# Optimization experiments

Hardware: AMD Instinct MI355X
Metric: run time of the kernel (lower is better)

## Reference

```python
import jax, jax.numpy as jnp
import numpy as np

DT = 0.1
DX = 1.0
DY = 1.0
NUM_STEPS = 5
EPS = 1e-06


def _smooth3(c):
    # replicate-pad 3-tap mean filter along last axis (matches F.pad replicate + conv1d)
    cp = jnp.concatenate([c[..., :1], c, c[..., -1:]], axis=-1)
    return (cp[..., :-2] + cp[..., 1:-1] + cp[..., 2:]) / 3.0


def _thomas(a, b, c, d):
    # a, b, c, d: (M, N). Batched Thomas solve, sequential recurrence over N via lax.scan.
    M, N = d.shape
    a0 = a.at[:, 0].set(0.0)  # a[:,0] unused; zero it so the first scan step gives c0/(b0+eps)

    def fwd(carry, inp):
        c_prev, d_prev = carry
        ai, bi, ci, di = inp
        denom = bi - ai * c_prev + EPS
        cs = ci / denom
        ds = (di - ai * d_prev) / denom
        return (cs, ds), (cs, ds)

    init = (jnp.zeros((M,), d.dtype), jnp.zeros((M,), d.dtype))
    _, (c_star, d_star) = jax.lax.scan(fwd, init, (a0.T, b.T, c.T, d.T))  # (N, M)

    def bwd(x_next, inp):
        cs, ds = inp
        x = ds - cs * x_next
        return x, x

    x_last = d_star[-1]
    _, x_rest = jax.lax.scan(bwd, x_last, (c_star[:-1], d_star[:-1]), reverse=True)
    x = jnp.concatenate([x_rest, x_last[None, :]], axis=0)  # (N, M)
    return x.T


def _diffuse_rows(u2, coef2, dt, dh):
    # u2, coef2: (M, N) rows solved independently
    cs = _smooth3(coef2) * dt / (dh * dh)
    a = -cs
    c = -cs
    b = 1.0 + 2.0 * cs
    b = b.at[:, 0].set(1.0 + cs[:, 0])
    b = b.at[:, -1].set(1.0 + cs[:, -1])
    return _thomas(a, b, c, u2)


def _coef_at(base, tcoef, t):
    return jnp.clip(base + tcoef * t, EPS, None)


def _forward(u, alpha_base, beta_base, alpha_time_coeff, beta_time_coeff):
    B, C, H, W = u.shape
    t = 0.0
    for _ in range(NUM_STEPS):
        # half step in x
        alpha = _coef_at(alpha_base, alpha_time_coeff, t)  # (C,H,W)
        af = jnp.broadcast_to(alpha[None], (B, C, H, W)).reshape(B * C * H, W)
        u = _diffuse_rows(u.reshape(B * C * H, W), af, DT / 2, DX).reshape(B, C, H, W)
        t += DT / 2
        # full step in y (transpose H<->W)
        beta = _coef_at(beta_base, beta_time_coeff, t)
        ut = jnp.swapaxes(u, 2, 3).reshape(B * C * W, H)
        bf = jnp.broadcast_to(jnp.swapaxes(beta, 1, 2)[None], (B, C, W, H)).reshape(B * C * W, H)
        ut = _diffuse_rows(ut, bf, DT, DY).reshape(B, C, W, H)
        u = jnp.swapaxes(ut, 2, 3)
        t += DT / 2
        # half step in x
        alpha = _coef_at(alpha_base, alpha_time_coeff, t)
        af = jnp.broadcast_to(alpha[None], (B, C, H, W)).reshape(B * C * H, W)
        u = _diffuse_rows(u.reshape(B * C * H, W), af, DT / 2, DX).reshape(B, C, H, W)
    return u


def setup_inputs() -> dict:
    key = jax.random.key(0)
    k1, k2, k3, k4, k5 = jax.random.split(key, 5)
    B, C, S = 2048, 3, 32
    u = jax.random.normal(k1, (B, C, S, S), dtype=jnp.float32)
    alpha_base = 1.0 + 0.1 * jax.random.normal(k2, (C, S, S), dtype=jnp.float32)
    beta_base = 1.0 + 0.1 * jax.random.normal(k3, (C, S, S), dtype=jnp.float32)
    alpha_time_coeff = 0.05 * jax.random.normal(k4, (C, S, S), dtype=jnp.float32)
    beta_time_coeff = 0.05 * jax.random.normal(k5, (C, S, S), dtype=jnp.float32)
    return {"u": u, "alpha_base": alpha_base, "beta_base": beta_base,
            "alpha_time_coeff": alpha_time_coeff, "beta_time_coeff": beta_time_coeff}


def reference(u, alpha_base, beta_base, alpha_time_coeff, beta_time_coeff):
    return _forward(u, alpha_base, beta_base, alpha_time_coeff, beta_time_coeff)
```

## Files before the change

kernel.cpp:

```cpp
#include <hip/hip_runtime.h>

static constexpr float EPSF = 1e-6f;


__global__ __launch_bounds__(64) void coef_kernel(
    const float* __restrict__ alpha_base, const float* __restrict__ beta_base,
    const float* __restrict__ alpha_tc,   const float* __restrict__ beta_tc,
    float4* __restrict__ C4)
{
    int gid  = blockIdx.x * 64 + threadIdx.x;
    int pair = gid >> 5;
    int ln   = gid & 31;
    if (pair >= 33) return;
    int set = pair / 3;
    int ch  = pair % 3;
    bool isX = (set < 6);
    float t  = isX ? 0.1f * (float)set : 0.1f * (float)(set - 6) + 0.05f;
    float dt = isX ? 0.05f : 0.1f;

    const float* bp; const float* tp; int stride;
    if (isX) { bp = alpha_base + (ch * 32 + ln) * 32; tp = alpha_tc + (ch * 32 + ln) * 32; stride = 1; }
    else     { bp = beta_base  + ch * 1024 + ln;      tp = beta_tc  + ch * 1024 + ln;      stride = 32; }

    float c[32];
    #pragma unroll
    for (int i = 0; i < 32; ++i)
        c[i] = fmaxf(fmaf(tp[i * stride], t, bp[i * stride]), EPSF);

    float cs[32];
    #pragma unroll
    for (int i = 0; i < 32; ++i) {
        float l = (i == 0)  ? c[0]  : c[i - 1];
        float r = (i == 31) ? c[31] : c[i + 1];
        cs[i] = (l + c[i] + r) / 3.0f * dt;
    }

    float p[32], sn[32];
    {
        float den = (1.0f + cs[0]) + EPSF;
        p[0]  = 1.0f / den;
        sn[0] = cs[0] * p[0];
        float sprev = -sn[0];
        #pragma unroll
        for (int i = 1; i < 32; ++i) {
            float bi = (i == 31) ? (1.0f + cs[31]) : fmaf(2.0f, cs[i], 1.0f);
            float ai = -cs[i];
            float dd = (bi - ai * sprev) + EPSF;
            float pi = 1.0f / dd;
            p[i]  = pi;
            float si = ai * pi;
            sn[i] = -si;
            sprev = si;
        }
    }

    float4* o = C4 + (set * 3 + ch) * 512 + ln;
    #pragma unroll
    for (int kk = 0; kk < 16; ++kk)
        o[kk * 32] = make_float4(p[2 * kk], sn[2 * kk], p[2 * kk + 1], sn[2 * kk + 1]);
}

__device__ __forceinline__ void loadc4(float p[32], float sn[32],
                                       const float4* __restrict__ c)
{
    #pragma unroll
    for (int kk = 0; kk < 16; ++kk) {
        float4 v = c[kk * 32];
        p[2 * kk]      = v.x; sn[2 * kk]     = v.y;
        p[2 * kk + 1]  = v.z; sn[2 * kk + 1] = v.w;
    }
}

__device__ __forceinline__ void solve2(float2 d[32], const float p[32], const float sn[32])
{
    float2 prev;
    prev.x = d[0].x * p[0];
    prev.y = d[0].y * p[0];
    d[0] = prev;
    #pragma unroll
    for (int i = 1; i < 32; ++i) {
        prev.x = fmaf(sn[i], prev.x, d[i].x * p[i]);
        prev.y = fmaf(sn[i], prev.y, d[i].y * p[i]);
        d[i] = prev;
    }
    #pragma unroll
    for (int i = 30; i >= 0; --i) {
        d[i].x = fmaf(sn[i], d[i + 1].x, d[i].x);
        d[i].y = fmaf(sn[i], d[i + 1].y, d[i].y);
    }
}

__global__ __launch_bounds__(64, 1) void diff_kernel(
    const float* __restrict__ u_in, float* __restrict__ u_out,
    const float4* __restrict__ C4, int blocksPerCh)
{
    __shared__ float4 tile4[2 * 546];
    const int l   = threadIdx.x;
    const int bid = blockIdx.x;
    const int ch  = bid / blocksPerCh;
    const int b0  = (bid % blocksPerCh) * 4;
    const int h   = l >> 5;
    const int ln  = l & 31;

    const int bA = b0 + h * 2;
    const float4* gA = reinterpret_cast<const float4*>(u_in + (bA * 3 + ch) * 1024);
    const float4* gB = gA + 768;
    float4* T4 = tile4 + h * 546;
    float2* T2 = reinterpret_cast<float2*>(T4);

    const float4* cb = C4 + ch * 512 + ln;
    float p[32], sn[32];
    loadc4(p, sn, cb);
    __builtin_amdgcn_sched_barrier(0);

    const int srow = ln >> 3, schk = ln & 7;
    #pragma unroll
    for (int r = 0; r < 8; ++r) {
        const int row = r * 4 + srow;
        float4 a = gA[row * 8 + schk];
        float4 b = gB[row * 8 + schk];
        float4* dst = T4 + row * 17 + 2 * schk;
        dst[0] = make_float4(a.x, b.x, a.y, b.y);
        dst[1] = make_float4(a.z, b.z, a.w, b.w);
    }

    float2 d[32];
    #pragma unroll
    for (int j = 0; j < 16; ++j) {
        float4 v = T4[ln * 17 + j];
        d[2 * j]     = make_float2(v.x, v.y);
        d[2 * j + 1] = make_float2(v.z, v.w);
    }
    solve2(d, p, sn);

    const float4* cy = cb + 6 * 1536;
    const float4* cx = cb + 1 * 1536;

    for (int step = 0; step < 5; ++step) {
        loadc4(p, sn, cy); cy += 1536;
        __builtin_amdgcn_sched_barrier(0);
        #pragma unroll
        for (int j = 0; j < 16; ++j)
            T4[ln * 17 + j] =
                make_float4(d[2 * j].x, d[2 * j].y, d[2 * j + 1].x, d[2 * j + 1].y);
        #pragma unroll
        for (int i = 0; i < 32; ++i)
            d[i] = T2[i * 34 + ln];
        solve2(d, p, sn);

        loadc4(p, sn, cx); cx += 1536;
        __builtin_amdgcn_sched_barrier(0);
        #pragma unroll
        for (int i = 0; i < 32; ++i)
            T2[i * 34 + ln] = d[i];
        #pragma unroll
        for (int j = 0; j < 16; ++j) {
            float4 v = T4[ln * 17 + j];
            d[2 * j]     = make_float2(v.x, v.y);
            d[2 * j + 1] = make_float2(v.z, v.w);
        }
        solve2(d, p, sn);
        if (step < 4) solve2(d, p, sn);
    }

    #pragma unroll
    for (int j = 0; j < 16; ++j)
        T4[ln * 17 + j] =
            make_float4(d[2 * j].x, d[2 * j].y, d[2 * j + 1].x, d[2 * j + 1].y);
    float4* oA = reinterpret_cast<float4*>(u_out + (bA * 3 + ch) * 1024);
    float4* oB = oA + 768;
    #pragma unroll
    for (int r = 0; r < 8; ++r) {
        const int row = r * 4 + srow;
        const float4* src = T4 + row * 17 + 2 * schk;
        float4 c0 = src[0], c1 = src[1];
        oA[row * 8 + schk] = make_float4(c0.x, c0.z, c1.x, c1.z);
        oB[row * 8 + schk] = make_float4(c0.y, c0.w, c1.y, c1.w);
    }
}

extern "C" void kernel_launch(void* const* d_in, const int* in_sizes, int n_in,
                              void* d_out, int out_size, void* d_ws, size_t ws_size,
                              hipStream_t stream)
{
    const float* u   = (const float*)d_in[0];
    const float* ab  = (const float*)d_in[1];
    const float* bb  = (const float*)d_in[2];
    const float* atc = (const float*)d_in[3];
    const float* btc = (const float*)d_in[4];
    float* out = (float*)d_out;
    float4* C4 = (float4*)d_ws;

    const int B = in_sizes[0] / (3 * 32 * 32);
    const int blocksPerCh = B / 4;

    coef_kernel<<<17, 64, 0, stream>>>(ab, bb, atc, btc, C4);
    diff_kernel<<<3 * blocksPerCh, 64, 0, stream>>>(u, out, C4, blocksPerCh);
}
```

Before: 102.0 us.

## Solve four batch images per thread instead of two in diffusion kernel

Each thread now carries four independent tridiagonal systems (float4) instead of two, so every block handles 8 batch elements and the grid is halved. The per-step coefficient loads and shared-memory traffic are spread over twice as many systems, and wider float4 shared accesses replace the float2 packing. The cost is twice the register footprint for the data array (128 floats) and larger shared tiles, which could cause spills or reduce occupancy. Halving the grid also leaves fewer blocks to hide latency.

```diff
diff --git a/kernel.cpp b/kernel.cpp
--- a/kernel.cpp
+++ b/kernel.cpp
@@ -71,22 +71,28 @@
     }
 }
 
-__device__ __forceinline__ void solve2(float2 d[32], const float p[32], const float sn[32])
-{
-    float2 prev;
+__device__ __forceinline__ void solve4(float4 d[32], const float p[32], const float sn[32])
+{
+    float4 prev;
     prev.x = d[0].x * p[0];
     prev.y = d[0].y * p[0];
+    prev.z = d[0].z * p[0];
+    prev.w = d[0].w * p[0];
     d[0] = prev;
     #pragma unroll
     for (int i = 1; i < 32; ++i) {
         prev.x = fmaf(sn[i], prev.x, d[i].x * p[i]);
         prev.y = fmaf(sn[i], prev.y, d[i].y * p[i]);
+        prev.z = fmaf(sn[i], prev.z, d[i].z * p[i]);
+        prev.w = fmaf(sn[i], prev.w, d[i].w * p[i]);
         d[i] = prev;
     }
     #pragma unroll
     for (int i = 30; i >= 0; --i) {
         d[i].x = fmaf(sn[i], d[i + 1].x, d[i].x);
         d[i].y = fmaf(sn[i], d[i + 1].y, d[i].y);
+        d[i].z = fmaf(sn[i], d[i + 1].z, d[i].z);
+        d[i].w = fmaf(sn[i], d[i + 1].w, d[i].w);
     }
 }
 
@@ -94,19 +100,20 @@
     const float* __restrict__ u_in, float* __restrict__ u_out,
     const float4* __restrict__ C4, int blocksPerCh)
 {
-    __shared__ float4 tile4[2 * 546];
+    __shared__ float4 tile4[2 * 1058];
     const int l   = threadIdx.x;
     const int bid = blockIdx.x;
     const int ch  = bid / blocksPerCh;
-    const int b0  = (bid % blocksPerCh) * 4;
+    const int b0  = (bid % blocksPerCh) * 8;
     const int h   = l >> 5;
     const int ln  = l & 31;
 
-    const int bA = b0 + h * 2;
+    const int bA = b0 + h * 4;
     const float4* gA = reinterpret_cast<const float4*>(u_in + (bA * 3 + ch) * 1024);
     const float4* gB = gA + 768;
-    float4* T4 = tile4 + h * 546;
-    float2* T2 = reinterpret_cast<float2*>(T4);
+    const float4* gC = gA + 1536;
+    const float4* gD = gA + 2304;
+    float4* T4 = tile4 + h * 1058;
 
     const float4* cb = C4 + ch * 512 + ln;
     float p[32], sn[32];
@@ -119,19 +126,20 @@
         const int row = r * 4 + srow;
         float4 a = gA[row * 8 + schk];
         float4 b = gB[row * 8 + schk];
-        float4* dst = T4 + row * 17 + 2 * schk;
-        dst[0] = make_float4(a.x, b.x, a.y, b.y);
-        dst[1] = make_float4(a.z, b.z, a.w, b.w);
-    }
-
-    float2 d[32];
-    #pragma unroll
-    for (int j = 0; j < 16; ++j) {
-        float4 v = T4[ln * 17 + j];
-        d[2 * j]     = make_float2(v.x, v.y);
-        d[2 * j + 1] = make_float2(v.z, v.w);
-    }
-    solve2(d, p, sn);
+        float4 c = gC[row * 8 + schk];
+        float4 e = gD[row * 8 + schk];
+        float4* dst = T4 + row * 33 + 4 * schk;
+        dst[0] = make_float4(a.x, b.x, c.x, e.x);
+        dst[1] = make_float4(a.y, b.y, c.y, e.y);
+        dst[2] = make_float4(a.z, b.z, c.z, e.z);
+        dst[3] = make_float4(a.w, b.w, c.w, e.w);
+    }
+
+    float4 d[32];
+    #pragma unroll
+    for (int j = 0; j < 32; ++j)
+        d[j] = T4[ln * 33 + j];
+    solve4(d, p, sn);
 
     const float4* cy = cb + 6 * 1536;
     const float4* cx = cb + 1 * 1536;
@@ -140,42 +148,41 @@
         loadc4(p, sn, cy); cy += 1536;
         __builtin_amdgcn_sched_barrier(0);
         #pragma unroll
-        for (int j = 0; j < 16; ++j)
-            T4[ln * 17 + j] =
-                make_float4(d[2 * j].x, d[2 * j].y, d[2 * j + 1].x, d[2 * j + 1].y);
+        for (int j = 0; j < 32; ++j)
+            T4[ln * 33 + j] = d[j];
         #pragma unroll
         for (int i = 0; i < 32; ++i)
-            d[i] = T2[i * 34 + ln];
-        solve2(d, p, sn);
+            d[i] = T4[i * 33 + ln];
+        solve4(d, p, sn);
 
         loadc4(p, sn, cx); cx += 1536;
         __builtin_amdgcn_sched_barrier(0);
         #pragma unroll
         for (int i = 0; i < 32; ++i)
-            T2[i * 34 + ln] = d[i];
-        #pragma unroll
-        for (int j = 0; j < 16; ++j) {
-            float4 v = T4[ln * 17 + j];
-            d[2 * j]     = make_float2(v.x, v.y);
-            d[2 * j + 1] = make_float2(v.z, v.w);
-        }
-        solve2(d, p, sn);
-        if (step < 4) solve2(d, p, sn);
-    }
-
-    #pragma unroll
-    for (int j = 0; j < 16; ++j)
-        T4[ln * 17 + j] =
-            make_float4(d[2 * j].x, d[2 * j].y, d[2 * j + 1].x, d[2 * j + 1].y);
+            T4[i * 33 + ln] = d[i];
+        #pragma unroll
+        for (int j = 0; j < 32; ++j)
+            d[j] = T4[ln * 33 + j];
+        solve4(d, p, sn);
+        if (step < 4) solve4(d, p, sn);
+    }
+
+    #pragma unroll
+    for (int j = 0; j < 32; ++j)
+        T4[ln * 33 + j] = d[j];
     float4* oA = reinterpret_cast<float4*>(u_out + (bA * 3 + ch) * 1024);
     float4* oB = oA + 768;
+    float4* oC = oA + 1536;
+    float4* oD = oA + 2304;
     #pragma unroll
     for (int r = 0; r < 8; ++r) {
         const int row = r * 4 + srow;
-        const float4* src = T4 + row * 17 + 2 * schk;
-        float4 c0 = src[0], c1 = src[1];
-        oA[row * 8 + schk] = make_float4(c0.x, c0.z, c1.x, c1.z);
-        oB[row * 8 + schk] = make_float4(c0.y, c0.w, c1.y, c1.w);
+        const float4* src = T4 + row * 33 + 4 * schk;
+        float4 c0 = src[0], c1 = src[1], c2 = src[2], c3 = src[3];
+        oA[row * 8 + schk] = make_float4(c0.x, c1.x, c2.x, c3.x);
+        oB[row * 8 + schk] = make_float4(c0.y, c1.y, c2.y, c3.y);
+        oC[row * 8 + schk] = make_float4(c0.z, c1.z, c2.z, c3.z);
+        oD[row * 8 + schk] = make_float4(c0.w, c1.w, c2.w, c3.w);
     }
 }
 
@@ -192,7 +199,7 @@
     float4* C4 = (float4*)d_ws;
 
     const int B = in_sizes[0] / (3 * 32 * 32);
-    const int blocksPerCh = B / 4;
+    const int blocksPerCh = B / 8;
 
     coef_kernel<<<17, 64, 0, stream>>>(ab, bb, atc, btc, C4);
     diff_kernel<<<3 * blocksPerCh, 64, 0, stream>>>(u, out, C4, blocksPerCh);
```

Measured after the change: 105.3 us. 3.2% more time.
